# Performance work log

Measured on AMD Instinct MI355X. Metric: run time of the kernel, lower is better.

Reference implementation:

```python
import jax, jax.numpy as jnp
from jax import lax
import numpy as np

EPS = 1e-8
NUM_ROUTES = 1152  # 32 * 6 * 6
NUM_OBJ = 10
OBJ_DIM = 16
PC_CAPS = 8
PC_CH = 32


def _squash(s, axis=-1):
    sq = jnp.sum(s * s, axis=axis, keepdims=True)
    return (sq / (1.0 + sq)) * s / jnp.sqrt(sq + EPS)


def setup_inputs() -> dict:
    key = jax.random.key(0)
    ks = jax.random.split(key, 12)
    B = 512
    image = jax.random.uniform(ks[0], (B, 1, 28, 28), dtype=jnp.float32)
    label = jax.random.randint(ks[1], (B,), 0, NUM_OBJ)
    conv_w = jax.random.normal(ks[2], (256, 1, 9, 9), dtype=jnp.float32) * 0.05
    conv_b = jnp.zeros((256,), jnp.float32)
    pc_w = jax.random.normal(ks[3], (PC_CAPS, PC_CH, 256, 9, 9), dtype=jnp.float32) * 0.02
    pc_b = jnp.zeros((PC_CAPS, PC_CH), jnp.float32)
    W_route = jax.random.normal(ks[4], (NUM_ROUTES, NUM_OBJ, OBJ_DIM, PC_CAPS), dtype=jnp.float32)
    dec_w1 = jax.random.normal(ks[5], (512, NUM_OBJ * OBJ_DIM), dtype=jnp.float32) * 0.05
    dec_b1 = jnp.zeros((512,), jnp.float32)
    dec_w2 = jax.random.normal(ks[6], (1024, 512), dtype=jnp.float32) * 0.05
    dec_b2 = jnp.zeros((1024,), jnp.float32)
    dec_w3 = jax.random.normal(ks[7], (784, 1024), dtype=jnp.float32) * 0.05
    dec_b3 = jnp.zeros((784,), jnp.float32)
    return {"image": image, "label": label, "conv_w": conv_w, "conv_b": conv_b,
            "pc_w": pc_w, "pc_b": pc_b, "W_route": W_route,
            "dec_w1": dec_w1, "dec_b1": dec_b1, "dec_w2": dec_w2, "dec_b2": dec_b2,
            "dec_w3": dec_w3, "dec_b3": dec_b3}


def reference(image, label, conv_w, conv_b, pc_w, pc_b, W_route,
              dec_w1, dec_b1, dec_w2, dec_b2, dec_w3, dec_b3):
    B = image.shape[0]
    # ConvEncoder: [B,1,28,28] -> [B,256,20,20]
    x = lax.conv_general_dilated(image, conv_w, (1, 1), 'VALID',
                                 dimension_numbers=('NCHW', 'OIHW', 'NCHW'))
    x = jax.nn.relu(x + conv_b[None, :, None, None])
    # PrimaryCaps: 8 parallel convs fused into one conv with 8*32 out channels
    pw = pc_w.reshape(PC_CAPS * PC_CH, 256, 9, 9)
    u = lax.conv_general_dilated(x, pw, (2, 2), 'VALID',
                                 dimension_numbers=('NCHW', 'OIHW', 'NCHW'))
    u = u + pc_b.reshape(-1)[None, :, None, None]  # [B,256,6,6] == stack dim=1 of [B,8,32,6,6]
    # faithful torch .view: [B,8,32,6,6] row-major -> [B,1152,8]
    u = u.reshape(B, NUM_ROUTES, PC_CAPS)
    u = _squash(u, axis=-1)
    # ObjectCaps dynamic routing
    # u_hat[b,r,j,o] = sum_c W[r,j,o,c] * u[b,r,c]
    u_hat = jnp.einsum('rjoc,brc->brjo', W_route, u)  # [B,1152,10,16]
    b_ij = jnp.zeros((B, NUM_ROUTES, NUM_OBJ), u_hat.dtype)
    v = None
    for it in range(3):
        c_ij = jax.nn.softmax(b_ij, axis=2)                  # softmax over capsules j
        s_j = jnp.einsum('brj,brjo->bjo', c_ij, u_hat)       # [B,10,16]
        v = _squash(s_j, axis=-1)
        if it < 2:
            b_ij = b_ij + jnp.einsum('brjo,bjo->brj', u_hat, v)
    obj_vectors = v[..., None]  # [B,10,16,1]
    # safe_norm over dim=2, squeeze(-1)
    y_prob = jnp.sqrt(jnp.sum(v * v, axis=-1) + EPS)  # [B,10]
    # Decoder: mask by label one-hot, MLP to reconstruction
    mask = jax.nn.one_hot(label, NUM_OBJ, dtype=v.dtype)
    masked = (v * mask[:, :, None]).reshape(B, NUM_OBJ * OBJ_DIM)
    h = jax.nn.relu(masked @ dec_w1.T + dec_b1)
    h = jax.nn.relu(h @ dec_w2.T + dec_b2)
    recon = jax.nn.sigmoid(h @ dec_w3.T + dec_b3).reshape(B, 1, 28, 28)
    return obj_vectors, recon, y_prob
```

## Files before the change

kernel.cpp:

```cpp
#include <hip/hip_runtime.h>
#include <hip/hip_bf16.h>

#define EPSF 1e-8f

typedef __attribute__((ext_vector_type(8))) short short8v;
typedef __attribute__((ext_vector_type(4))) float float4v;

static __device__ __forceinline__ unsigned short f2bf_bits(float x)
{
    return __builtin_bit_cast(unsigned short, __float2bfloat16(x));
}

__global__ __launch_bounds__(256) void k_bw2(const float* __restrict__ pw,
                                             __hip_bfloat16* __restrict__ Bw2)
{
    const int oc = blockIdx.x;
    const int t = threadIdx.x;
    __shared__ unsigned short wl[20736];
    for (int i = t; i < 20736; i += 256)
        wl[i] = f2bf_bits(pw[(size_t)oc * 20736 + i]);
    __syncthreads();
    const int r16 = oc & 15, nt = (oc >> 4) & 3, wcq = oc >> 6;
    for (int e = t; e < 2592; e += 256) {
        const int kidx = e >> 5, icc = (e >> 2) & 7, slot = e & 3;
        short8v v;
        #pragma unroll
        for (int i = 0; i < 8; ++i)
            v[i] = (short)wl[(icc * 32 + slot * 8 + i) * 81 + kidx];
        const int chunk = ((kidx * 8 + icc) * 4 + wcq) * 4 + nt;
        *(short8v*)(Bw2 + (size_t)chunk * 512 + (slot * 16 + r16) * 8) = v;
    }
}

__global__ __launch_bounds__(256) void k_conv1(const float* __restrict__ img,
                                               const float* __restrict__ cw,
                                               const float* __restrict__ cb,
                                               __hip_bfloat16* __restrict__ xt)
{
    const int b = blockIdx.x;
    const int c = threadIdx.x;
    __shared__ float simg[784];
    for (int i = c; i < 784; i += 256) simg[i] = img[b * 784 + i];
    float wreg[81];
    const float* wp = cw + c * 81;
    #pragma unroll
    for (int k = 0; k < 81; ++k) wreg[k] = wp[k];
    const float bias = cb[c];
    __syncthreads();

    const int icc = c >> 5, slot = (c >> 3) & 3, ic8 = c & 7;
    char* xbase = (char*)xt + ((size_t)b * 8 + icc) * 25600;

    for (int wg = 0; wg < 5; ++wg) {
        const float* base = &simg[wg * 4];
        float win[9][12];
        #pragma unroll
        for (int r = 0; r < 8; ++r) {
            const float4v* rp = (const float4v*)(base + r * 28);
            float4v A = rp[0], B = rp[1], C = rp[2];
            win[r][0] = A.x; win[r][1] = A.y; win[r][2]  = A.z; win[r][3]  = A.w;
            win[r][4] = B.x; win[r][5] = B.y; win[r][6]  = B.z; win[r][7]  = B.w;
            win[r][8] = C.x; win[r][9] = C.y; win[r][10] = C.z; win[r][11] = C.w;
        }
        #pragma unroll
        for (int h = 0; h < 20; ++h) {
            {
                const int ws = (h + 8) % 9;
                const float4v* rp = (const float4v*)(base + (h + 8) * 28);
                float4v A = rp[0], B = rp[1], C = rp[2];
                win[ws][0] = A.x; win[ws][1] = A.y; win[ws][2]  = A.z; win[ws][3]  = A.w;
                win[ws][4] = B.x; win[ws][5] = B.y; win[ws][6]  = B.z; win[ws][7]  = B.w;
                win[ws][8] = C.x; win[ws][9] = C.y; win[ws][10] = C.z; win[ws][11] = C.w;
            }
            float acc[4] = {bias, bias, bias, bias};
            #pragma unroll
            for (int ky = 0; ky < 9; ++ky) {
                const int rs = (h + ky) % 9;
                #pragma unroll
                for (int kx = 0; kx < 9; ++kx) {
                    const float wv = wreg[ky * 9 + kx];
                    #pragma unroll
                    for (int i = 0; i < 4; ++i)
                        acc[i] = fmaf(win[rs][kx + i], wv, acc[i]);
                }
            }
            #pragma unroll
            for (int i = 0; i < 4; ++i) {
                int w = wg * 4 + i;
                float av = fmaxf(acc[i], 0.f);
                int pos = h * 20 + (w & 1) * 10 + (w >> 1);
                int off = pos * 64 + ((slot ^ ((pos >> 1) & 3)) << 4) + ic8 * 2;
                *(unsigned short*)(xbase + off) = f2bf_bits(av);
            }
        }
    }
}

__device__ __forceinline__ void stage_x(const __hip_bfloat16* __restrict__ xt,
                                        char* dst, int b0, int icc, int t)
{
    const __hip_bfloat16* base0 = xt + ((size_t)(b0    ) * 8 + icc) * 12800;
    const __hip_bfloat16* base1 = xt + ((size_t)(b0 + 1) * 8 + icc) * 12800;
    #pragma unroll
    for (int k = 0; k < 12; ++k) {
        const int unit = t + k * 256;
        const __hip_bfloat16* gp = (unit < 1600) ? (base0 + unit * 8)
                                                 : (base1 + (unit - 1600) * 8);
        __builtin_amdgcn_global_load_lds(
            (const __attribute__((address_space(1))) unsigned int*)gp,
            (__attribute__((address_space(3))) unsigned int*)(dst + unit * 16),
            16, 0, 0);
    }
    if (t < 128) {
        const int unit = 3072 + t;
        const __hip_bfloat16* gp = base1 + (unit - 1600) * 8;
        __builtin_amdgcn_global_load_lds(
            (const __attribute__((address_space(1))) unsigned int*)gp,
            (__attribute__((address_space(3))) unsigned int*)(dst + unit * 16),
            16, 0, 0);
    }
}

__global__ __launch_bounds__(256, 2) void k_conv2(const __hip_bfloat16* __restrict__ xt,
                                                  const __hip_bfloat16* __restrict__ Bw2,
                                                  const float* __restrict__ pcb,
                                                  float* __restrict__ u0,
                                                  float* __restrict__ u1)
{
    const int pair = blockIdx.x >> 1;
    const int ks = blockIdx.x & 1;
    const int b0 = pair * 2;
    const int t = threadIdx.x;
    const int lane = t & 63, wc = t >> 6;
    const int r16 = lane & 15, slot = lane >> 4;

    __shared__ alignas(16) char xs[51200];

    int aimg[5], lc[5];
    #pragma unroll
    for (int mt = 0; mt < 5; ++mt) {
        int grow = mt * 16 + r16;
        int img = (grow >= 36 && grow < 72) ? 1 : 0;
        int hw = (grow < 72) ? (grow - 36 * img) : 0;
        int h = hw / 6, w = hw - h * 6;
        aimg[mt] = img * 25600;
        lc[mt] = 40 * h + w;
    }

    float4v acc[5][4];
    #pragma unroll
    for (int mt = 0; mt < 5; ++mt)
        #pragma unroll
        for (int nt = 0; nt < 4; ++nt)
            acc[mt][nt] = (float4v){0.f, 0.f, 0.f, 0.f};

    for (int i4 = 0; i4 < 4; ++i4) {
        const int icc = ks * 4 + i4;
        __syncthreads();
        stage_x(xt, xs, b0, icc, t);
        __syncthreads();

        const __hip_bfloat16* bp = Bw2 + ((size_t)icc * 4 + wc) * 2048 + lane * 8;

        #pragma unroll 3
        for (int kidx = 0; kidx < 81; ++kidx) {
            int ky = kidx / 9, kx = kidx - ky * 9;
            int scalK = 20 * ky + 10 * (kx & 1) + (kx >> 1);
            short8v a[5];
            #pragma unroll
            for (int mt = 0; mt < 5; ++mt) {
                int pos = lc[mt] + scalK;
                int off = aimg[mt] + pos * 64 + (((slot ^ (pos >> 1)) & 3) << 4);
                a[mt] = *(const short8v*)(xs + off);
            }
            const __hip_bfloat16* bq = bp + (size_t)kidx * 65536;
            short8v bv[4];
            #pragma unroll
            for (int nt = 0; nt < 4; ++nt)
                bv[nt] = *(const short8v*)(bq + nt * 512);
            #pragma unroll
            for (int mt = 0; mt < 5; ++mt)
                #pragma unroll
                for (int nt = 0; nt < 4; ++nt)
                    acc[mt][nt] = __builtin_amdgcn_mfma_f32_16x16x32_bf16(a[mt], bv[nt], acc[mt][nt], 0, 0, 0);
        }
    }

    float* uo = ks ? u1 : u0;
    #pragma unroll
    for (int mt = 0; mt < 5; ++mt) {
        int grow0 = mt * 16 + slot * 4;
        if (grow0 < 72) {
            int img = grow0 >= 36;
            int hwb = grow0 - 36 * img;
            const int b = b0 + img;
            #pragma unroll
            for (int nt = 0; nt < 4; ++nt) {
                int oc = wc * 64 + nt * 16 + r16;
                float pb = ks ? 0.f : pcb[oc];
                float4v v = acc[mt][nt];
                v.x += pb; v.y += pb; v.z += pb; v.w += pb;
                *(float4v*)(uo + (size_t)b * 9216 + oc * 36 + hwb) = v;
            }
        }
    }
}

__global__ void k_squash_u2(float* __restrict__ u0, const float* __restrict__ u1,
                            int ngroups)
{
    int g = blockIdx.x * blockDim.x + threadIdx.x;
    if (g >= ngroups) return;
    float4v* p0 = (float4v*)(u0 + (size_t)g * 8);
    const float4v* p1 = (const float4v*)(u1 + (size_t)g * 8);
    float4v a = p0[0] + p1[0], c = p0[1] + p1[1];
    float sq = a.x * a.x + a.y * a.y + a.z * a.z + a.w * a.w
             + c.x * c.x + c.y * c.y + c.z * c.z + c.w * c.w;
    float scale = (sq / (1.f + sq)) / sqrtf(sq + EPSF);
    a *= scale; c *= scale;
    p0[0] = a; p0[1] = c;
}

__global__ __launch_bounds__(256, 2) void k_route3(const float* __restrict__ u,
                                                   const float* __restrict__ W,
                                                   const float* __restrict__ vsum,
                                                   float* __restrict__ spart, int iter)
{
    const int bid = blockIdx.x;
    const int rc = bid % 144;
    const int bc = bid / 144;
    const int r0 = rc * 8;
    const int b0 = bc * 128;
    const int t = threadIdx.x;
    const int oq = t & 3;
    const int img = t >> 2;
    const int bA = b0 + img, bB = bA + 64;

    __shared__ alignas(16) float Wl[10240];
    __shared__ alignas(16) float ul[128 * 68];

    #pragma unroll
    for (int k = 0; k < 10; ++k) {
        int e = t + k * 256;
        int rr = e / 320, rest = e - rr * 320;
        float4v val = *(const float4v*)(W + (size_t)(r0 + rr) * 1280 + rest * 4);
        int es = e ^ ((e >> 3) & 3);
        *(float4v*)(Wl + es * 4) = val;
    }
    #pragma unroll
    for (int k = 0; k < 8; ++k) {
        int e = t + k * 256;
        int im = e >> 4, f4 = e & 15;
        float4v val = *(const float4v*)(u + (size_t)(b0 + im) * 9216 + rc * 64 + f4 * 4);
        *(float4v*)(ul + im * 68 + f4 * 4) = val;
    }
    __syncthreads();

    float4v accA[10], accB[10];
    #pragma unroll
    for (int j = 0; j < 10; ++j) {
        accA[j] = (float4v){0.f, 0.f, 0.f, 0.f};
        accB[j] = (float4v){0.f, 0.f, 0.f, 0.f};
    }

    const float* upA = ul + img * 68;
    const float* upB = ul + (img + 64) * 68;

    for (int r = 0; r < 8; ++r) {
        float4v uA0 = *(const float4v*)(upA + r * 8);
        float4v uA1 = *(const float4v*)(upA + r * 8 + 4);
        float4v uB0 = *(const float4v*)(upB + r * 8);
        float4v uB1 = *(const float4v*)(upB + r * 8 + 4);
        float4v uhA[10], uhB[10];
        #pragma unroll
        for (int j = 0; j < 10; ++j) {
            #pragma unroll
            for (int oo = 0; oo < 4; ++oo) {
                int un = r * 320 + j * 32 + oq * 8 + oo * 2;
                int i0 = un ^ oq;
                int i1 = i0 ^ 1;
                float4v wlo = *(const float4v*)(Wl + i0 * 4);
                float4v whi = *(const float4v*)(Wl + i1 * 4);
                uhA[j][oo] = wlo.x * uA0.x + wlo.y * uA0.y + wlo.z * uA0.z + wlo.w * uA0.w
                           + whi.x * uA1.x + whi.y * uA1.y + whi.z * uA1.z + whi.w * uA1.w;
                uhB[j][oo] = wlo.x * uB0.x + wlo.y * uB0.y + wlo.z * uB0.z + wlo.w * uB0.w
                           + whi.x * uB1.x + whi.y * uB1.y + whi.z * uB1.z + whi.w * uB1.w;
            }
        }
        if (iter > 0) {
            #pragma unroll 2
            for (int half = 0; half < 2; ++half) {
                const int b = half ? bB : bA;
                float4v* uh = half ? uhB : uhA;
                float4v* acc = half ? accB : accA;
                float q[10];
                #pragma unroll
                for (int j = 0; j < 10; ++j) {
                    float4v vj = *(const float4v*)(vsum + (size_t)b * 160 + j * 16 + oq * 4);
                    float qp = uh[j].x * vj.x + uh[j].y * vj.y
                             + uh[j].z * vj.z + uh[j].w * vj.w;
                    qp += __shfl_xor(qp, 1);
                    qp += __shfl_xor(qp, 2);
                    q[j] = qp;
                }
                float mx = q[0];
                #pragma unroll
                for (int j = 1; j < 10; ++j) mx = fmaxf(mx, q[j]);
                float ssum = 0.f;
                float c[10];
                #pragma unroll
                for (int j = 0; j < 10; ++j) { c[j] = __expf(q[j] - mx); ssum += c[j]; }
                float inv = 1.f / ssum;
                #pragma unroll
                for (int j = 0; j < 10; ++j) acc[j] += (c[j] * inv) * uh[j];
            }
        } else {
            #pragma unroll
            for (int j = 0; j < 10; ++j) {
                accA[j] += 0.1f * uhA[j];
                accB[j] += 0.1f * uhB[j];
            }
        }
    }

    float* dstA = spart + ((size_t)rc * 512 + bA) * 160 + oq * 4;
    float* dstB = spart + ((size_t)rc * 512 + bB) * 160 + oq * 4;
    #pragma unroll
    for (int j = 0; j < 10; ++j) {
        *(float4v*)(dstA + j * 16) = accA[j];
        *(float4v*)(dstB + j * 16) = accB[j];
    }
}

__global__ void k_finish(const float* __restrict__ spart, float* __restrict__ vsum,
                         const int* __restrict__ label, float* __restrict__ obj,
                         float* __restrict__ yprob, float* __restrict__ masked, int iter)
{
    const int b = blockIdx.x, t = threadIdx.x;
    if (t < 160) {
        const float* sp = spart + (size_t)b * 160 + t;
        float sv = 0.f;
        #pragma unroll 8
        for (int rc = 0; rc < 144; ++rc)
            sv += sp[(size_t)rc * 81920];
        float sq = sv * sv;
        sq += __shfl_xor(sq, 1); sq += __shfl_xor(sq, 2);
        sq += __shfl_xor(sq, 4); sq += __shfl_xor(sq, 8);
        float v = sv * (sq / (1.f + sq)) / sqrtf(sq + EPSF);
        float pv = (iter > 0) ? vsum[b * 160 + t] : 0.f;
        vsum[b * 160 + t] = pv + v;
        if (iter == 2) {
            obj[b * 160 + t] = v;
            float vv = v * v;
            vv += __shfl_xor(vv, 1); vv += __shfl_xor(vv, 2);
            vv += __shfl_xor(vv, 4); vv += __shfl_xor(vv, 8);
            int j = t >> 4;
            if ((t & 15) == 0) yprob[b * 10 + j] = sqrtf(vv + EPSF);
            masked[b * 160 + t] = (label[b] == j) ? v : 0.f;
        }
    }
}

__global__ void k_mlp(const float* __restrict__ A, const float* __restrict__ Wt,
                      const float* __restrict__ bias, float* __restrict__ C,
                      int N, int K, int act)
{
    const int m0 = blockIdx.x * 32;
    const int n0 = blockIdx.y * 32;
    const int t  = threadIdx.x;
    const int tn = t & 31, tg = t >> 5;
    __shared__ float As[32][33];
    __shared__ float Ws[32][33];
    float acc[4] = {0.f, 0.f, 0.f, 0.f};
    for (int k0 = 0; k0 < K; k0 += 32) {
        __syncthreads();
        for (int idx = t; idx < 1024; idx += 256) {
            int rr = idx >> 5, kk = idx & 31;
            As[rr][kk] = A[(size_t)(m0 + rr) * K + k0 + kk];
            int n = n0 + rr;
            Ws[rr][kk] = (n < N) ? Wt[(size_t)n * K + k0 + kk] : 0.f;
        }
        __syncthreads();
        #pragma unroll 8
        for (int kk = 0; kk < 32; ++kk) {
            float bv = Ws[tn][kk];
            #pragma unroll
            for (int i = 0; i < 4; ++i)
                acc[i] += As[tg * 4 + i][kk] * bv;
        }
    }
    int n = n0 + tn;
    if (n < N) {
        float bs = bias[n];
        #pragma unroll
        for (int i = 0; i < 4; ++i) {
            float vv = acc[i] + bs;
            vv = (act == 0) ? fmaxf(vv, 0.f) : 1.f / (1.f + expf(-vv));
            C[(size_t)(m0 + tg * 4 + i) * N + n] = vv;
        }
    }
}

extern "C" void kernel_launch(void* const* d_in, const int* in_sizes, int n_in,
                              void* d_out, int out_size, void* d_ws, size_t ws_size,
                              hipStream_t stream)
{
    const float* image  = (const float*)d_in[0];
    const int*   label  = (const int*)  d_in[1];
    const float* conv_w = (const float*)d_in[2];
    const float* conv_b = (const float*)d_in[3];
    const float* pc_w   = (const float*)d_in[4];
    const float* pc_b   = (const float*)d_in[5];
    const float* Wrt    = (const float*)d_in[6];
    const float* dw1 = (const float*)d_in[7];
    const float* db1 = (const float*)d_in[8];
    const float* dw2 = (const float*)d_in[9];
    const float* db2 = (const float*)d_in[10];
    const float* dw3 = (const float*)d_in[11];
    const float* db3 = (const float*)d_in[12];
    float* out = (float*)d_out;

    char* p = (char*)d_ws;
    __hip_bfloat16* xt  = (__hip_bfloat16*)p; p += 104857600;
    float* u      = (float*)p; p += 18874368;
    float* u1     = (float*)p; p += 18874368;
    __hip_bfloat16* Bw2 = (__hip_bfloat16*)p; p += 10616832;
    float* vsum   = (float*)p; p += 327680;
    float* masked = (float*)p; p += 327680;
    float* h1     = (float*)p; p += 1048576;
    float* h2     = (float*)p; p += 2097152;

    float* spart = (float*)xt;

    float* obj   = out;
    float* recon = out + 81920;
    float* yprob = out + 483328;

    k_bw2<<<256, 256, 0, stream>>>(pc_w, Bw2);
    k_conv1<<<512, 256, 0, stream>>>(image, conv_w, conv_b, xt);
    k_conv2<<<512, 256, 0, stream>>>(xt, Bw2, pc_b, u, u1);
    k_squash_u2<<<2304, 256, 0, stream>>>(u, u1, 589824);
    for (int it = 0; it < 3; ++it) {
        k_route3<<<576, 256, 0, stream>>>(u, Wrt, vsum, spart, it);
        k_finish<<<512, 192, 0, stream>>>(spart, vsum, label, obj, yprob, masked, it);
    }
    k_mlp<<<dim3(16, 16), 256, 0, stream>>>(masked, dw1, db1, h1, 512, 160, 0);
    k_mlp<<<dim3(16, 32), 256, 0, stream>>>(h1, dw2, db2, h2, 1024, 512, 0);
    k_mlp<<<dim3(16, 25), 256, 0, stream>>>(h2, dw3, db3, recon, 784, 1024, 1);
}
```

Baseline: 695.7 us.

## Fuse squash into routing loads and use label-gathered first decoder layer

The split-K partial sums and squash of the primary capsules are now done while k_route3 loads u into shared memory, which removes the separate k_squash_u2 kernel and its read-write pass over u. Because that load happens on every routing iteration, the squash is recomputed three times and both partial buffers are read each time. The first decoder layer is replaced by a kernel that gathers only the label's 16-element capsule slice and its matching weight columns. This skips the masked zero entries and the masked buffer.

After: 693.4 us. Within noise of the previous version (-0.3%).

```diff
diff --git a/kernel.cpp b/kernel.cpp
--- a/kernel.cpp
+++ b/kernel.cpp
@@ -206,22 +206,8 @@
     }
 }
 
-__global__ void k_squash_u2(float* __restrict__ u0, const float* __restrict__ u1,
-                            int ngroups)
-{
-    int g = blockIdx.x * blockDim.x + threadIdx.x;
-    if (g >= ngroups) return;
-    float4v* p0 = (float4v*)(u0 + (size_t)g * 8);
-    const float4v* p1 = (const float4v*)(u1 + (size_t)g * 8);
-    float4v a = p0[0] + p1[0], c = p0[1] + p1[1];
-    float sq = a.x * a.x + a.y * a.y + a.z * a.z + a.w * a.w
-             + c.x * c.x + c.y * c.y + c.z * c.z + c.w * c.w;
-    float scale = (sq / (1.f + sq)) / sqrtf(sq + EPSF);
-    a *= scale; c *= scale;
-    p0[0] = a; p0[1] = c;
-}
-
-__global__ __launch_bounds__(256, 2) void k_route3(const float* __restrict__ u,
+__global__ __launch_bounds__(256, 2) void k_route3(const float* __restrict__ u0,
+                                                   const float* __restrict__ u1,
                                                    const float* __restrict__ W,
                                                    const float* __restrict__ vsum,
                                                    float* __restrict__ spart, int iter)
@@ -248,11 +234,20 @@
         *(float4v*)(Wl + es * 4) = val;
     }
     #pragma unroll
-    for (int k = 0; k < 8; ++k) {
+    for (int k = 0; k < 4; ++k) {
         int e = t + k * 256;
-        int im = e >> 4, f4 = e & 15;
-        float4v val = *(const float4v*)(u + (size_t)(b0 + im) * 9216 + rc * 64 + f4 * 4);
-        *(float4v*)(ul + im * 68 + f4 * 4) = val;
+        int im = e >> 3, cap = e & 7;
+        size_t gb = (size_t)(b0 + im) * 9216 + rc * 64 + cap * 8;
+        const float4v* pA = (const float4v*)(u0 + gb);
+        const float4v* pB = (const float4v*)(u1 + gb);
+        float4v a = pA[0] + pB[0];
+        float4v c = pA[1] + pB[1];
+        float sq = a.x * a.x + a.y * a.y + a.z * a.z + a.w * a.w
+                 + c.x * c.x + c.y * c.y + c.z * c.z + c.w * c.w;
+        float scale = (sq / (1.f + sq)) / sqrtf(sq + EPSF);
+        a *= scale; c *= scale;
+        *(float4v*)(ul + im * 68 + cap * 8) = a;
+        *(float4v*)(ul + im * 68 + cap * 8 + 4) = c;
     }
     __syncthreads();
 
@@ -333,8 +328,7 @@
 }
 
 __global__ void k_finish(const float* __restrict__ spart, float* __restrict__ vsum,
-                         const int* __restrict__ label, float* __restrict__ obj,
-                         float* __restrict__ yprob, float* __restrict__ masked, int iter)
+                         float* __restrict__ obj, float* __restrict__ yprob, int iter)
 {
     const int b = blockIdx.x, t = threadIdx.x;
     if (t < 160) {
@@ -354,9 +348,42 @@
             float vv = v * v;
             vv += __shfl_xor(vv, 1); vv += __shfl_xor(vv, 2);
             vv += __shfl_xor(vv, 4); vv += __shfl_xor(vv, 8);
-            int j = t >> 4;
-            if ((t & 15) == 0) yprob[b * 10 + j] = sqrtf(vv + EPSF);
-            masked[b * 160 + t] = (label[b] == j) ? v : 0.f;
+            if ((t & 15) == 0) yprob[b * 10 + (t >> 4)] = sqrtf(vv + EPSF);
+        }
+    }
+}
+
+__global__ __launch_bounds__(256) void k_mlp1g(const float* __restrict__ obj,
+                                               const int* __restrict__ label,
+                                               const float* __restrict__ w1,
+                                               const float* __restrict__ b1,
+                                               float* __restrict__ h1)
+{
+    const int b0 = blockIdx.x * 8;
+    const int t = threadIdx.x;
+    __shared__ float vl[8][16];
+    __shared__ int labs[8];
+    if (t < 8) labs[t] = label[b0 + t];
+    __syncthreads();
+    if (t < 128) {
+        int m = t >> 4, o = t & 15;
+        vl[m][o] = obj[(size_t)(b0 + m) * 160 + labs[m] * 16 + o];
+    }
+    __syncthreads();
+    #pragma unroll 2
+    for (int nn = 0; nn < 2; ++nn) {
+        const int n = t + nn * 256;
+        const float bs = b1[n];
+        #pragma unroll
+        for (int m = 0; m < 8; ++m) {
+            const float4v* wp = (const float4v*)(w1 + (size_t)n * 160 + labs[m] * 16);
+            float4v w0 = wp[0], w1v = wp[1], w2 = wp[2], w3 = wp[3];
+            float q = bs;
+            q += vl[m][0]  * w0.x  + vl[m][1]  * w0.y  + vl[m][2]  * w0.z  + vl[m][3]  * w0.w;
+            q += vl[m][4]  * w1v.x + vl[m][5]  * w1v.y + vl[m][6]  * w1v.z + vl[m][7]  * w1v.w;
+            q += vl[m][8]  * w2.x  + vl[m][9]  * w2.y  + vl[m][10] * w2.z  + vl[m][11] * w2.w;
+            q += vl[m][12] * w3.x  + vl[m][13] * w3.y  + vl[m][14] * w3.z  + vl[m][15] * w3.w;
+            h1[(size_t)(b0 + m) * 512 + n] = fmaxf(q, 0.f);
         }
     }
 }
@@ -426,7 +453,6 @@
     float* u1     = (float*)p; p += 18874368;
     __hip_bfloat16* Bw2 = (__hip_bfloat16*)p; p += 10616832;
     float* vsum   = (float*)p; p += 327680;
-    float* masked = (float*)p; p += 327680;
     float* h1     = (float*)p; p += 1048576;
     float* h2     = (float*)p; p += 2097152;
 
@@ -439,12 +465,11 @@
     k_bw2<<<256, 256, 0, stream>>>(pc_w, Bw2);
     k_conv1<<<512, 256, 0, stream>>>(image, conv_w, conv_b, xt);
     k_conv2<<<512, 256, 0, stream>>>(xt, Bw2, pc_b, u, u1);
-    k_squash_u2<<<2304, 256, 0, stream>>>(u, u1, 589824);
     for (int it = 0; it < 3; ++it) {
-        k_route3<<<576, 256, 0, stream>>>(u, Wrt, vsum, spart, it);
-        k_finish<<<512, 192, 0, stream>>>(spart, vsum, label, obj, yprob, masked, it);
-    }
-    k_mlp<<<dim3(16, 16), 256, 0, stream>>>(masked, dw1, db1, h1, 512, 160, 0);
+        k_route3<<<576, 256, 0, stream>>>(u, u1, Wrt, vsum, spart, it);
+        k_finish<<<512, 192, 0, stream>>>(spart, vsum, obj, yprob, it);
+    }
+    k_mlp1g<<<64, 256, 0, stream>>>(obj, label, dw1, db1, h1);
     k_mlp<<<dim3(16, 32), 256, 0, stream>>>(h1, dw2, db2, h2, 1024, 512, 0);
     k_mlp<<<dim3(16, 25), 256, 0, stream>>>(h2, dw3, db3, recon, 784, 1024, 1);
 }
```
